# Kernel optimization log

Measured on AMD Instinct MI355X. Metric: run time of the kernel, lower is better.

## Reference

```python
import jax, jax.numpy as jnp
import numpy as np


def setup_inputs() -> dict:
    key = jax.random.key(0)
    k1, k2 = jax.random.split(key)
    B, S, H, E = 2, 4096, 5120, 64
    hidden_states = jax.random.normal(k1, (B, S, H), dtype=jnp.float32)
    weight = jax.random.normal(k2, (E, H), dtype=jnp.float32) * (1.0 / np.sqrt(H))
    e_score_correction_bias = jnp.zeros((E,), dtype=jnp.float32)
    return {
        "hidden_states": hidden_states,
        "weight": weight,
        "e_score_correction_bias": e_score_correction_bias,
        "top_k": 8,
    }


def reference(hidden_states, weight, e_score_correction_bias, top_k):
    H = hidden_states.shape[-1]
    x = hidden_states.reshape(-1, H)                      # [T, H]
    logits = jnp.einsum("th,eh->te", x, weight) + e_score_correction_bias  # [T, E]
    topk_logits, topk_idx = jax.lax.top_k(logits, top_k)  # [T, K] each
    topk_weight = jax.nn.softmax(topk_logits, axis=-1)    # [T, K]
    return topk_idx, topk_weight
```

## Files before the change

kernel.cpp:

```cpp
#include <hip/hip_runtime.h>
#include <hip/hip_bf16.h>
#include <math.h>

#define TOK  8192
#define NE   64
#define NH   5120
#define TOPK 8
#define NTG  (TOK / 64)
#define NP   (NE * NH / 2)
#define LOGN (TOK * NE)
#define NKB  (NH / 32)

typedef __attribute__((ext_vector_type(8))) short bf16x8;
typedef __attribute__((ext_vector_type(4))) float f32x4;

union Frag { unsigned int u[4]; bf16x8 v; };

__device__ __forceinline__ void split3_2(float x0, float x1,
    unsigned int& hi, unsigned int& mid, unsigned int& lo)
{
    unsigned int u0 = __float_as_uint(x0), u1 = __float_as_uint(x1);
    float h0 = __uint_as_float(u0 & 0xffff0000u);
    float h1 = __uint_as_float(u1 & 0xffff0000u);
    hi = __builtin_amdgcn_perm(u1, u0, 0x07060302u);
    float r0 = x0 - h0, r1 = x1 - h1;
    unsigned int m0u = __float_as_uint(r0) & 0xffff0000u;
    unsigned int m1u = __float_as_uint(r1) & 0xffff0000u;
    mid = __builtin_amdgcn_perm(m1u, m0u, 0x07060302u);
    float l0 = r0 - __uint_as_float(m0u);
    float l1 = r1 - __uint_as_float(m1u);
    unsigned int v0 = __float_as_uint(l0) + 0x8000u;
    unsigned int v1 = __float_as_uint(l1) + 0x8000u;
    lo = __builtin_amdgcn_perm(v1, v0, 0x07060302u);
}

__global__ __launch_bounds__(256) void wsplit_k(const float* __restrict__ w,
                                                unsigned int* __restrict__ whl)
{
    const int t  = blockIdx.x * 256 + threadIdx.x;
    const int k8 = t % (NH / 8);
    const int e  = t / (NH / 8);
    const int kb = k8 >> 2;
    const int kg = k8 & 3;

    const float4* xp = reinterpret_cast<const float4*>(w + (size_t)e * NH + k8 * 8);
    const float4 a = xp[0], b = xp[1];

    uint4 h, m, l;
    split3_2(a.x, a.y, h.x, m.x, l.x);
    split3_2(a.z, a.w, h.y, m.y, l.y);
    split3_2(b.x, b.y, h.z, m.z, l.z);
    split3_2(b.z, b.w, h.w, m.w, l.w);

    const size_t o = (size_t)kb * 1024 + kg * 256 + e * 4;
    *reinterpret_cast<uint4*>(whl + o)          = h;
    *reinterpret_cast<uint4*>(whl + NP + o)     = m;
    *reinterpret_cast<uint4*>(whl + 2 * NP + o) = l;
}

template <int KSPLIT>
__global__ __launch_bounds__(256, 4) void gemm_k(
    const float* __restrict__ x, const unsigned int* __restrict__ whl,
    float* __restrict__ part)
{
    constexpr int KLEN = NH / KSPLIT;
    const int lane = threadIdx.x & 63;
    const int wv   = threadIdx.x >> 6;
    const int tg   = blockIdx.x;
    const int ks   = blockIdx.y;
    const int arow = lane & 15;
    const int kg   = lane >> 4;

    const float* xrow = x + (size_t)(tg * 64 + wv * 16 + arow) * NH
                          + ks * KLEN + kg * 8;
    const unsigned int* wb0 = whl + (size_t)(ks * (KLEN / 32)) * 1024
                                  + kg * 256 + arow * 4;

    f32x4 acc[4];
#pragma unroll
    for (int n = 0; n < 4; ++n) acc[n] = (f32x4){0.f, 0.f, 0.f, 0.f};

    for (int kk = 0; kk < KLEN / 32; ++kk) {
        const float4 a0 = *reinterpret_cast<const float4*>(xrow + kk * 32);
        const float4 a1 = *reinterpret_cast<const float4*>(xrow + kk * 32 + 4);
        Frag ah, am, al;
        split3_2(a0.x, a0.y, ah.u[0], am.u[0], al.u[0]);
        split3_2(a0.z, a0.w, ah.u[1], am.u[1], al.u[1]);
        split3_2(a1.x, a1.y, ah.u[2], am.u[2], al.u[2]);
        split3_2(a1.z, a1.w, ah.u[3], am.u[3], al.u[3]);
        const unsigned int* wk = wb0 + (size_t)kk * 1024;
#pragma unroll
        for (int n = 0; n < 4; ++n) {
            Frag bh, bm, bl;
            *reinterpret_cast<int4*>(bh.u) =
                *reinterpret_cast<const int4*>(wk + n * 64);
            *reinterpret_cast<int4*>(bm.u) =
                *reinterpret_cast<const int4*>(wk + NP + n * 64);
            *reinterpret_cast<int4*>(bl.u) =
                *reinterpret_cast<const int4*>(wk + 2 * NP + n * 64);
            acc[n] = __builtin_amdgcn_mfma_f32_16x16x32_bf16(ah.v, bh.v, acc[n], 0, 0, 0);
            acc[n] = __builtin_amdgcn_mfma_f32_16x16x32_bf16(am.v, bh.v, acc[n], 0, 0, 0);
            acc[n] = __builtin_amdgcn_mfma_f32_16x16x32_bf16(ah.v, bm.v, acc[n], 0, 0, 0);
            acc[n] = __builtin_amdgcn_mfma_f32_16x16x32_bf16(am.v, bm.v, acc[n], 0, 0, 0);
            acc[n] = __builtin_amdgcn_mfma_f32_16x16x32_bf16(al.v, bh.v, acc[n], 0, 0, 0);
            acc[n] = __builtin_amdgcn_mfma_f32_16x16x32_bf16(ah.v, bl.v, acc[n], 0, 0, 0);
        }
    }

    float* pb = part + (((size_t)ks * NTG + tg) * 64) * 64;
#pragma unroll
    for (int n = 0; n < 4; ++n)
#pragma unroll
        for (int i = 0; i < 4; ++i) {
            const int tokl = wv * 16 + kg * 4 + i;
            const int e    = n * 16 + arow;
            pb[(size_t)tokl * 64 + e] = acc[n][i];
        }
}

__global__ __launch_bounds__(256) void reduce_k(
    float4* __restrict__ part4, const float4* __restrict__ bias4, int nks)
{
    const int i = blockIdx.x * 256 + threadIdx.x;
    float4 acc = bias4[i & 15];
    for (int p = 0; p < nks; ++p) {
        const float4 v = part4[(size_t)p * (LOGN / 4) + i];
        acc.x += v.x; acc.y += v.y; acc.z += v.z; acc.w += v.w;
    }
    part4[i] = acc;
}

__global__ __launch_bounds__(64) void topk_k(
    const float* __restrict__ logits, float* __restrict__ out)
{
    const int t = blockIdx.x * 64 + (threadIdx.x & 63);

    float acc[NE];
    const float4* lp = reinterpret_cast<const float4*>(logits + (size_t)t * NE);
#pragma unroll
    for (int e4 = 0; e4 < 16; ++e4) {
        const float4 v = lp[e4];
        acc[e4 * 4 + 0] = v.x; acc[e4 * 4 + 1] = v.y;
        acc[e4 * 4 + 2] = v.z; acc[e4 * 4 + 3] = v.w;
    }

    float vals[TOPK]; int idxs[TOPK];
#pragma unroll
    for (int k = 0; k < TOPK; ++k) {
        float m = -INFINITY; int mi = 0;
#pragma unroll
        for (int e = 0; e < NE; ++e) {
            const bool b = acc[e] > m;
            m  = b ? acc[e] : m;
            mi = b ? e  : mi;
        }
        vals[k] = m; idxs[k] = mi;
#pragma unroll
        for (int e = 0; e < NE; ++e)
            acc[e] = (e == mi) ? -INFINITY : acc[e];
    }

    float wts[TOPK];
    float s = 0.f;
#pragma unroll
    for (int k = 0; k < TOPK; ++k) { wts[k] = __expf(vals[k] - vals[0]); s += wts[k]; }
    const float inv = 1.f / s;
#pragma unroll
    for (int k = 0; k < TOPK; ++k) wts[k] *= inv;

    float4 i0, i1, w0, w1;
    i0.x = (float)idxs[0]; i0.y = (float)idxs[1]; i0.z = (float)idxs[2]; i0.w = (float)idxs[3];
    i1.x = (float)idxs[4]; i1.y = (float)idxs[5]; i1.z = (float)idxs[6]; i1.w = (float)idxs[7];
    w0.x = wts[0]; w0.y = wts[1]; w0.z = wts[2]; w0.w = wts[3];
    w1.x = wts[4]; w1.y = wts[5]; w1.z = wts[6]; w1.w = wts[7];

    float* oi = out + (size_t)t * TOPK;
    float* ow = out + (size_t)TOK * TOPK + (size_t)t * TOPK;
    *reinterpret_cast<float4*>(oi)     = i0;
    *reinterpret_cast<float4*>(oi + 4) = i1;
    *reinterpret_cast<float4*>(ow)     = w0;
    *reinterpret_cast<float4*>(ow + 4) = w1;
}

extern "C" void kernel_launch(void* const* d_in, const int* in_sizes, int n_in,
                              void* d_out, int out_size, void* d_ws, size_t ws_size,
                              hipStream_t stream)
{
    const float* x    = (const float*)d_in[0];
    const float* w    = (const float*)d_in[1];
    const float* bias = (const float*)d_in[2];
    float* out = (float*)d_out;

    const size_t whl_bytes = (size_t)3 * NP * sizeof(unsigned int);
    const size_t part16    = (size_t)16 * LOGN * sizeof(float);
    const int KS = (ws_size >= part16 + whl_bytes) ? 16 : 8;

    float*        part = (float*)d_ws;
    unsigned int* whl  = (unsigned int*)((char*)d_ws
                         + (size_t)KS * LOGN * sizeof(float));

    wsplit_k<<<dim3((NE * NH / 8) / 256), 256, 0, stream>>>(w, whl);
    if (KS == 16)
        gemm_k<16><<<dim3(NTG, 16), 256, 0, stream>>>(x, whl, part);
    else
        gemm_k<8><<<dim3(NTG, 8), 256, 0, stream>>>(x, whl, part);
    reduce_k<<<dim3(LOGN / 4 / 256), 256, 0, stream>>>(
        (float4*)part, (const float4*)bias, KS);
    topk_k<<<dim3(NTG), 64, 0, stream>>>(part, out);
}
```

Measured before the change: 299.0 us.

## Enlarge GEMM register tile to 64 tokens per wave and fuse reduce with top-k

Each wave now computes a 64x64 output tile (4x4 MFMA accumulators), so each weight fragment load is reused across four token sub-tiles. This reduces weight-fragment traffic per MFMA at the cost of many more accumulator registers and fewer blocks (32 x KS). The launch-bounds occupancy hint is dropped. The split-K reduction and top-k/softmax are merged into one kernel that stages logits in LDS, which removes one launch and a logits round-trip through global memory. Only 16 of 256 threads do the top-k selection.

```diff
diff --git a/kernel.cpp b/kernel.cpp
--- a/kernel.cpp
+++ b/kernel.cpp
@@ -6,10 +6,8 @@
 #define NE   64
 #define NH   5120
 #define TOPK 8
-#define NTG  (TOK / 64)
 #define NP   (NE * NH / 2)
 #define LOGN (TOK * NE)
-#define NKB  (NH / 32)
 
 typedef __attribute__((ext_vector_type(8))) short bf16x8;
 typedef __attribute__((ext_vector_type(4))) float f32x4;
@@ -59,7 +57,7 @@
 }
 
 template <int KSPLIT>
-__global__ __launch_bounds__(256, 4) void gemm_k(
+__global__ __launch_bounds__(256) void gemm_k(
     const float* __restrict__ x, const unsigned int* __restrict__ whl,
     float* __restrict__ part)
 {
@@ -71,115 +69,129 @@
     const int arow = lane & 15;
     const int kg   = lane >> 4;
 
-    const float* xrow = x + (size_t)(tg * 64 + wv * 16 + arow) * NH
-                          + ks * KLEN + kg * 8;
+    const int trow0 = tg * 256 + wv * 64;
+    const float* xbase = x + (size_t)trow0 * NH + ks * KLEN + kg * 8;
     const unsigned int* wb0 = whl + (size_t)(ks * (KLEN / 32)) * 1024
                                   + kg * 256 + arow * 4;
 
-    f32x4 acc[4];
-#pragma unroll
-    for (int n = 0; n < 4; ++n) acc[n] = (f32x4){0.f, 0.f, 0.f, 0.f};
-
+    f32x4 acc[4][4];
+#pragma unroll
+    for (int m = 0; m < 4; ++m)
+#pragma unroll
+        for (int n = 0; n < 4; ++n) acc[m][n] = (f32x4){0.f, 0.f, 0.f, 0.f};
+
+#pragma unroll 2
     for (int kk = 0; kk < KLEN / 32; ++kk) {
-        const float4 a0 = *reinterpret_cast<const float4*>(xrow + kk * 32);
-        const float4 a1 = *reinterpret_cast<const float4*>(xrow + kk * 32 + 4);
-        Frag ah, am, al;
-        split3_2(a0.x, a0.y, ah.u[0], am.u[0], al.u[0]);
-        split3_2(a0.z, a0.w, ah.u[1], am.u[1], al.u[1]);
-        split3_2(a1.x, a1.y, ah.u[2], am.u[2], al.u[2]);
-        split3_2(a1.z, a1.w, ah.u[3], am.u[3], al.u[3]);
         const unsigned int* wk = wb0 + (size_t)kk * 1024;
+        Frag bh[4], bm[4], bl[4];
 #pragma unroll
         for (int n = 0; n < 4; ++n) {
-            Frag bh, bm, bl;
-            *reinterpret_cast<int4*>(bh.u) =
+            *reinterpret_cast<int4*>(bh[n].u) =
                 *reinterpret_cast<const int4*>(wk + n * 64);
-            *reinterpret_cast<int4*>(bm.u) =
+            *reinterpret_cast<int4*>(bm[n].u) =
                 *reinterpret_cast<const int4*>(wk + NP + n * 64);
-            *reinterpret_cast<int4*>(bl.u) =
+            *reinterpret_cast<int4*>(bl[n].u) =
                 *reinterpret_cast<const int4*>(wk + 2 * NP + n * 64);
-            acc[n] = __builtin_amdgcn_mfma_f32_16x16x32_bf16(ah.v, bh.v, acc[n], 0, 0, 0);
-            acc[n] = __builtin_amdgcn_mfma_f32_16x16x32_bf16(am.v, bh.v, acc[n], 0, 0, 0);
-            acc[n] = __builtin_amdgcn_mfma_f32_16x16x32_bf16(ah.v, bm.v, acc[n], 0, 0, 0);
-            acc[n] = __builtin_amdgcn_mfma_f32_16x16x32_bf16(am.v, bm.v, acc[n], 0, 0, 0);
-            acc[n] = __builtin_amdgcn_mfma_f32_16x16x32_bf16(al.v, bh.v, acc[n], 0, 0, 0);
-            acc[n] = __builtin_amdgcn_mfma_f32_16x16x32_bf16(ah.v, bl.v, acc[n], 0, 0, 0);
+        }
+#pragma unroll
+        for (int m = 0; m < 4; ++m) {
+            const float* xr = xbase + (size_t)(m * 16 + arow) * NH + kk * 32;
+            const float4 a0 = *reinterpret_cast<const float4*>(xr);
+            const float4 a1 = *reinterpret_cast<const float4*>(xr + 4);
+            Frag ah, am_, al;
+            split3_2(a0.x, a0.y, ah.u[0], am_.u[0], al.u[0]);
+            split3_2(a0.z, a0.w, ah.u[1], am_.u[1], al.u[1]);
+            split3_2(a1.x, a1.y, ah.u[2], am_.u[2], al.u[2]);
+            split3_2(a1.z, a1.w, ah.u[3], am_.u[3], al.u[3]);
+#pragma unroll
+            for (int n = 0; n < 4; ++n) {
+                acc[m][n] = __builtin_amdgcn_mfma_f32_16x16x32_bf16(ah.v,  bh[n].v, acc[m][n], 0, 0, 0);
+                acc[m][n] = __builtin_amdgcn_mfma_f32_16x16x32_bf16(am_.v, bh[n].v, acc[m][n], 0, 0, 0);
+                acc[m][n] = __builtin_amdgcn_mfma_f32_16x16x32_bf16(ah.v,  bm[n].v, acc[m][n], 0, 0, 0);
+                acc[m][n] = __builtin_amdgcn_mfma_f32_16x16x32_bf16(am_.v, bm[n].v, acc[m][n], 0, 0, 0);
+                acc[m][n] = __builtin_amdgcn_mfma_f32_16x16x32_bf16(al.v,  bh[n].v, acc[m][n], 0, 0, 0);
+                acc[m][n] = __builtin_amdgcn_mfma_f32_16x16x32_bf16(ah.v,  bl[n].v, acc[m][n], 0, 0, 0);
+            }
         }
     }
 
-    float* pb = part + (((size_t)ks * NTG + tg) * 64) * 64;
-#pragma unroll
-    for (int n = 0; n < 4; ++n)
-#pragma unroll
-        for (int i = 0; i < 4; ++i) {
-            const int tokl = wv * 16 + kg * 4 + i;
-            const int e    = n * 16 + arow;
-            pb[(size_t)tokl * 64 + e] = acc[n][i];
+    float* pb = part + ((size_t)ks * TOK + trow0) * 64;
+#pragma unroll
+    for (int m = 0; m < 4; ++m)
+#pragma unroll
+        for (int n = 0; n < 4; ++n)
+#pragma unroll
+            for (int i = 0; i < 4; ++i) {
+                const int tokl = m * 16 + kg * 4 + i;
+                const int e    = n * 16 + arow;
+                pb[(size_t)tokl * 64 + e] = acc[m][n][i];
+            }
+}
+
+__global__ __launch_bounds__(256) void redtopk_k(
+    const float4* __restrict__ part4, const float4* __restrict__ bias4,
+    float* __restrict__ out, int nks)
+{
+    __shared__ float lds[16][65];
+    const int t   = threadIdx.x;
+    const int blk = blockIdx.x;
+
+    float4 acc4 = bias4[t & 15];
+    const size_t base = (size_t)blk * 256 + t;
+    for (int p = 0; p < nks; ++p) {
+        const float4 v = part4[(size_t)p * (LOGN / 4) + base];
+        acc4.x += v.x; acc4.y += v.y; acc4.z += v.z; acc4.w += v.w;
+    }
+    const int tok = t >> 4, eq = t & 15;
+    lds[tok][eq * 4 + 0] = acc4.x;
+    lds[tok][eq * 4 + 1] = acc4.y;
+    lds[tok][eq * 4 + 2] = acc4.z;
+    lds[tok][eq * 4 + 3] = acc4.w;
+    __syncthreads();
+
+    if (t < 16) {
+        float acc[NE];
+#pragma unroll
+        for (int e = 0; e < NE; ++e) acc[e] = lds[t][e];
+
+        float vals[TOPK]; int idxs[TOPK];
+#pragma unroll
+        for (int k = 0; k < TOPK; ++k) {
+            float m = -INFINITY; int mi = 0;
+#pragma unroll
+            for (int e = 0; e < NE; ++e) {
+                const bool b = acc[e] > m;
+                m  = b ? acc[e] : m;
+                mi = b ? e  : mi;
+            }
+            vals[k] = m; idxs[k] = mi;
+#pragma unroll
+            for (int e = 0; e < NE; ++e)
+                acc[e] = (e == mi) ? -INFINITY : acc[e];
         }
-}
-
-__global__ __launch_bounds__(256) void reduce_k(
-    float4* __restrict__ part4, const float4* __restrict__ bias4, int nks)
-{
-    const int i = blockIdx.x * 256 + threadIdx.x;
-    float4 acc = bias4[i & 15];
-    for (int p = 0; p < nks; ++p) {
-        const float4 v = part4[(size_t)p * (LOGN / 4) + i];
-        acc.x += v.x; acc.y += v.y; acc.z += v.z; acc.w += v.w;
+
+        float wts[TOPK];
+        float s = 0.f;
+#pragma unroll
+        for (int k = 0; k < TOPK; ++k) { wts[k] = __expf(vals[k] - vals[0]); s += wts[k]; }
+        const float inv = 1.f / s;
+#pragma unroll
+        for (int k = 0; k < TOPK; ++k) wts[k] *= inv;
+
+        float4 i0, i1, w0, w1;
+        i0.x = (float)idxs[0]; i0.y = (float)idxs[1]; i0.z = (float)idxs[2]; i0.w = (float)idxs[3];
+        i1.x = (float)idxs[4]; i1.y = (float)idxs[5]; i1.z = (float)idxs[6]; i1.w = (float)idxs[7];
+        w0.x = wts[0]; w0.y = wts[1]; w0.z = wts[2]; w0.w = wts[3];
+        w1.x = wts[4]; w1.y = wts[5]; w1.z = wts[6]; w1.w = wts[7];
+
+        const int token = blk * 16 + t;
+        float* oi = out + (size_t)token * TOPK;
+        float* ow = out + (size_t)TOK * TOPK + (size_t)token * TOPK;
+        *reinterpret_cast<float4*>(oi)     = i0;
+        *reinterpret_cast<float4*>(oi + 4) = i1;
+        *reinterpret_cast<float4*>(ow)     = w0;
+        *reinterpret_cast<float4*>(ow + 4) = w1;
     }
-    part4[i] = acc;
-}
-
-__global__ __launch_bounds__(64) void topk_k(
-    const float* __restrict__ logits, float* __restrict__ out)
-{
-    const int t = blockIdx.x * 64 + (threadIdx.x & 63);
-
-    float acc[NE];
-    const float4* lp = reinterpret_cast<const float4*>(logits + (size_t)t * NE);
-#pragma unroll
-    for (int e4 = 0; e4 < 16; ++e4) {
-        const float4 v = lp[e4];
-        acc[e4 * 4 + 0] = v.x; acc[e4 * 4 + 1] = v.y;
-        acc[e4 * 4 + 2] = v.z; acc[e4 * 4 + 3] = v.w;
-    }
-
-    float vals[TOPK]; int idxs[TOPK];
-#pragma unroll
-    for (int k = 0; k < TOPK; ++k) {
-        float m = -INFINITY; int mi = 0;
-#pragma unroll
-        for (int e = 0; e < NE; ++e) {
-            const bool b = acc[e] > m;
-            m  = b ? acc[e] : m;
-            mi = b ? e  : mi;
-        }
-        vals[k] = m; idxs[k] = mi;
-#pragma unroll
-        for (int e = 0; e < NE; ++e)
-            acc[e] = (e == mi) ? -INFINITY : acc[e];
-    }
-
-    float wts[TOPK];
-    float s = 0.f;
-#pragma unroll
-    for (int k = 0; k < TOPK; ++k) { wts[k] = __expf(vals[k] - vals[0]); s += wts[k]; }
-    const float inv = 1.f / s;
-#pragma unroll
-    for (int k = 0; k < TOPK; ++k) wts[k] *= inv;
-
-    float4 i0, i1, w0, w1;
-    i0.x = (float)idxs[0]; i0.y = (float)idxs[1]; i0.z = (float)idxs[2]; i0.w = (float)idxs[3];
-    i1.x = (float)idxs[4]; i1.y = (float)idxs[5]; i1.z = (float)idxs[6]; i1.w = (float)idxs[7];
-    w0.x = wts[0]; w0.y = wts[1]; w0.z = wts[2]; w0.w = wts[3];
-    w1.x = wts[4]; w1.y = wts[5]; w1.z = wts[6]; w1.w = wts[7];
-
-    float* oi = out + (size_t)t * TOPK;
-    float* ow = out + (size_t)TOK * TOPK + (size_t)t * TOPK;
-    *reinterpret_cast<float4*>(oi)     = i0;
-    *reinterpret_cast<float4*>(oi + 4) = i1;
-    *reinterpret_cast<float4*>(ow)     = w0;
-    *reinterpret_cast<float4*>(ow + 4) = w1;
 }
 
 extern "C" void kernel_launch(void* const* d_in, const int* in_sizes, int n_in,
@@ -201,10 +213,9 @@
 
     wsplit_k<<<dim3((NE * NH / 8) / 256), 256, 0, stream>>>(w, whl);
     if (KS == 16)
-        gemm_k<16><<<dim3(NTG, 16), 256, 0, stream>>>(x, whl, part);
+        gemm_k<16><<<dim3(TOK / 256, 16), 256, 0, stream>>>(x, whl, part);
     else
-        gemm_k<8><<<dim3(NTG, 8), 256, 0, stream>>>(x, whl, part);
-    reduce_k<<<dim3(LOGN / 4 / 256), 256, 0, stream>>>(
-        (float4*)part, (const float4*)bias, KS);
-    topk_k<<<dim3(NTG), 64, 0, stream>>>(part, out);
-}
+        gemm_k<8><<<dim3(TOK / 256, 8), 256, 0, stream>>>(x, whl, part);
+    redtopk_k<<<dim3(TOK / 16), 256, 0, stream>>>(
+        (const float4*)part, (const float4*)bias, out, KS);
+}
```

New measurement: 277.3 us. -7.3%, faster.
